# Kernel tuning notes

Measured on AMD Instinct MI355X. Metric: run time of the kernel, lower is better.

## Reference

```python
import jax, jax.numpy as jnp
import numpy as np

B, S, D = 4, 2048, 1024
H = 16
HD = D // H  # 64

def setup_inputs() -> dict:
    key = jax.random.key(0)
    ks = jax.random.split(key, 4)
    scale = 0.02
    return {
        "hidden_states": jax.random.normal(ks[0], (B, S, D), dtype=jnp.float32),
        "attention_mask": jnp.zeros((B, 1, 1, S), dtype=jnp.float32),
        "Wq": jax.random.normal(ks[1], (D, D), dtype=jnp.float32) * scale,
        "bq": jnp.zeros((D,), dtype=jnp.float32),
        "Wk": jax.random.normal(ks[2], (D, D), dtype=jnp.float32) * scale,
        "bk": jnp.zeros((D,), dtype=jnp.float32),
        "Wv": jax.random.normal(ks[3], (D, D), dtype=jnp.float32) * scale,
        "bv": jnp.zeros((D,), dtype=jnp.float32),
    }

def reference(hidden_states, attention_mask, Wq, bq, Wk, bk, Wv, bv):
    b, s, d = hidden_states.shape
    def proj(W, bias):
        # Linear then split heads: [b, s, d] -> [b, H, s, HD]
        y = hidden_states @ W.T + bias
        return y.reshape(b, s, H, HD).transpose(0, 2, 1, 3)
    Q = proj(Wq, bq)
    K = proj(Wk, bk)
    V = proj(Wv, bv)
    scores = jnp.einsum('bhqd,bhkd->bhqk', Q, K) / jnp.sqrt(jnp.float32(HD))
    scores = scores + attention_mask  # additive mask, broadcast [b,1,1,s]
    probs = jax.nn.softmax(scores, axis=-1)
    # dropout prob = 0.0 (eval-mode): identity
    context = jnp.einsum('bhqk,bhkd->bhqd', probs, V)
    return context.transpose(0, 2, 1, 3).reshape(b, s, d)
```

## Files before the change

### kernel.cpp

```cpp
#include <hip/hip_runtime.h>


typedef short bf16x4 __attribute__((ext_vector_type(4)));
typedef short bf16x8 __attribute__((ext_vector_type(8)));
typedef float f32x4 __attribute__((ext_vector_type(4)));

#define SEQ 2048
#define DIM 1024
#define NH 16
#define HDIM 64
#define QKV_ELEMS ((size_t)64 * SEQ * HDIM)

#define WS_FLAG  50331648ull
#define WS_XBF   50331904ull
#define WS_WBF   67109120ull
#define WS_BF32  73400576ull
#define WS_NEED  73412868ull

#define LOG2E 1.4426950408889634f
#define QSCALE (0.125f * LOG2E)

static __device__ __forceinline__ unsigned short f2bf(float f) {
  union { float f; unsigned u; } x; x.f = f;
  unsigned r = x.u + 0x7fffu + ((x.u >> 16) & 1u);
  return (unsigned short)(r >> 16);
}
static __device__ __forceinline__ float bf2f(unsigned short h) {
  union { unsigned u; float f; } x; x.u = ((unsigned)h) << 16;
  return x.f;
}
static __device__ __forceinline__ unsigned cvtpk(float a, float b) {
  unsigned r;
  asm("v_cvt_pk_bf16_f32 %0, %1, %2" : "=v"(r) : "v"(a), "v"(b));
  return r;
}
static __device__ __forceinline__ int vswz(int s) {
  return (s & ~31) | (((s >> 2) & 3) << 3) | (((s >> 4) & 1) << 2);
}
static __device__ __forceinline__ void vm_drain() {
  asm volatile("s_waitcnt vmcnt(0)" ::: "memory");
}

template <bool FP32>
static __device__ __forceinline__ float load1(const void* p, size_t i) {
  if (FP32) return ((const float*)p)[i];
  else      return bf2f(((const unsigned short*)p)[i]);
}
template <bool FP32>
static __device__ __forceinline__ bf16x8 load8bf(const void* p, size_t i) {
  if (FP32) {
    f32x4 a = *(const f32x4*)((const float*)p + i);
    f32x4 b = *(const f32x4*)((const float*)p + i + 4);
    union { bf16x8 v; unsigned short u[8]; } r;
#pragma unroll
    for (int j = 0; j < 4; ++j) { r.u[j] = f2bf(a[j]); r.u[4 + j] = f2bf(b[j]); }
    return r.v;
  } else {
    return *(const bf16x8*)((const unsigned short*)p + i);
  }
}
static __device__ __forceinline__ bf16x8 load8bf_rt(const void* p, size_t i, bool fp32) {
  return fp32 ? load8bf<true>(p, i) : load8bf<false>(p, i);
}

static __device__ __forceinline__ void glds16(const unsigned short* g, unsigned short* l) {
  __builtin_amdgcn_global_load_lds(
      (const __attribute__((address_space(1))) unsigned int*)(unsigned long long)(const void*)g,
      (__attribute__((address_space(3))) unsigned int*)(unsigned int)(unsigned long long)(void*)l,
      16, 0, 0);
}

__global__ void detect_dtype(const unsigned short* __restrict__ X, int* __restrict__ flag) {
  __shared__ int zc[1024], bc[1024];
  int z = 0, b = 0;
  for (int i = threadIdx.x; i < 4096; i += 1024) {
    unsigned short u = X[8 * i];
    if (u == 0) z++;
    int e = (u >> 7) & 0xff;
    if (e >= 134) b++;
  }
  zc[threadIdx.x] = z; bc[threadIdx.x] = b;
  __syncthreads();
  for (int s = 512; s > 0; s >>= 1) {
    if (threadIdx.x < s) { zc[threadIdx.x] += zc[threadIdx.x + s]; bc[threadIdx.x] += bc[threadIdx.x + s]; }
    __syncthreads();
  }
  if (threadIdx.x == 0)
    *flag = (zc[0] > 2048 || bc[0] > 16) ? 1 : 0;
}

__global__ void convert_all_u(const void* __restrict__ X,
                              const void* __restrict__ Wq, const void* __restrict__ Wk,
                              const void* __restrict__ Wv,
                              const void* __restrict__ bq, const void* __restrict__ bk,
                              const void* __restrict__ bv,
                              unsigned char* __restrict__ ws, const int* __restrict__ flag) {
  const bool fp32 = (*flag != 0);
  unsigned short* Xb = (unsigned short*)(ws + WS_XBF);
  unsigned short* Wb = (unsigned short*)(ws + WS_WBF);
  float* Bb = (float*)(ws + WS_BF32);
  int blk = blockIdx.x;
  if (blk < 4096) {
    size_t base = ((size_t)blk * 256 + threadIdx.x) * 8;
    *(bf16x8*)(Xb + base) = load8bf_rt(X, base, fp32);
  } else if (blk < 5632) {
    int w = (blk - 4096) >> 9;
    int r = (blk - 4096) & 511;
    const void* W = (w == 0) ? Wq : (w == 1) ? Wk : Wv;
    size_t base = ((size_t)r * 256 + threadIdx.x) * 8;
    *(bf16x8*)(Wb + (size_t)w * 1048576 + base) = load8bf_rt(W, base, fp32);
  } else {
    int w = blk - 5632;
    const void* Bsrc = (w == 0) ? bq : (w == 1) ? bk : bv;
    for (int i = threadIdx.x; i < 1024; i += 256)
      Bb[w * 1024 + i] = fp32 ? load1<true>(Bsrc, i) : load1<false>(Bsrc, i);
  }
}

__global__ __launch_bounds__(512, 2) void qkv_bf(
    const unsigned short* __restrict__ Xb, const unsigned short* __restrict__ Wb,
    const float* __restrict__ Bb,
    unsigned short* __restrict__ Qo, unsigned short* __restrict__ Ko,
    unsigned short* __restrict__ Vo)
{
  const int bid = blockIdx.x;
  const int wg  = (bid & 7) * 192 + (bid >> 3);
  const int z   = wg / 512;
  const int rem = wg - z * 512;
  const int nb  = rem >> 6;
  const int mb  = rem & 63;
  const unsigned short* W = Wb + (size_t)z * 1048576;

  __shared__ __align__(16) unsigned short Xs[2][128 * 64];
  __shared__ __align__(16) unsigned short Ws[2][128 * 64];

  const int tid  = threadIdx.x;
  const int wave = tid >> 6;
  const int lane = tid & 63;
  const int col  = lane & 15;
  const int quad = lane >> 4;
  const int wr = wave & 1;
  const int wc = wave >> 1;
  const int m0 = mb * 128;
  const int n0 = nb * 128;

  f32x4 zero4 = {0.f, 0.f, 0.f, 0.f};
  f32x4 acc[4][2];
#pragma unroll
  for (int i = 0; i < 4; ++i)
#pragma unroll
    for (int j = 0; j < 2; ++j) acc[i][j] = zero4;

  const int srow8 = lane >> 3;
  const int sseg  = lane & 7;
  const int lseg  = sseg ^ srow8;
  const unsigned short* xA0 = Xb + (size_t)(m0 + 0  + wave * 8 + srow8) * DIM + lseg * 8;
  const unsigned short* xA1 = Xb + (size_t)(m0 + 64 + wave * 8 + srow8) * DIM + lseg * 8;
  const unsigned short* wA0 = W  + (size_t)(n0 + 0  + wave * 8 + srow8) * DIM + lseg * 8;
  const unsigned short* wA1 = W  + (size_t)(n0 + 64 + wave * 8 + srow8) * DIM + lseg * 8;

  auto stage = [&](int k0, int bufn) {
    unsigned short* Xd = Xs[bufn] + (wave * 8) * 64;
    unsigned short* Wd = Ws[bufn] + (wave * 8) * 64;
    glds16(xA0 + k0, Xd);
    glds16(xA1 + k0, Xd + 64 * 64);
    glds16(wA0 + k0, Wd);
    glds16(wA1 + k0, Wd + 64 * 64);
  };

  stage(0, 0);

  if (z < 2) {
    for (int ks = 0; ks < 16; ++ks) {
      vm_drain();
      __syncthreads();
      if (ks < 15) stage((ks + 1) * 64, (ks + 1) & 1);
      const unsigned short* Xc = Xs[ks & 1];
      const unsigned short* Wc = Ws[ks & 1];
#pragma unroll
      for (int kk = 0; kk < 2; ++kk) {
        bf16x8 Af[4], Bf[2];
#pragma unroll
        for (int i = 0; i < 4; ++i) {
          int ra = wr * 64 + i * 16 + col;
          Af[i] = *(const bf16x8*)(Xc + ra * 64 + ((kk * 4 + quad) ^ (ra & 7)) * 8);
        }
#pragma unroll
        for (int j = 0; j < 2; ++j) {
          int rb = wc * 32 + j * 16 + col;
          Bf[j] = *(const bf16x8*)(Wc + rb * 64 + ((kk * 4 + quad) ^ (rb & 7)) * 8);
        }
#pragma unroll
        for (int i = 0; i < 4; ++i)
#pragma unroll
          for (int j = 0; j < 2; ++j)
            acc[i][j] = __builtin_amdgcn_mfma_f32_16x16x32_bf16(Bf[j], Af[i], acc[i][j], 0, 0, 0);
      }
    }

    const float oscale = (z == 0) ? QSCALE : 1.0f;
    unsigned short* Yo = (z == 0) ? Qo : Ko;
#pragma unroll
    for (int i = 0; i < 4; ++i) {
      int m = m0 + wr * 64 + i * 16 + col;
      int b = m >> 11, s = m & 2047;
#pragma unroll
      for (int j = 0; j < 2; ++j) {
        int n = n0 + wc * 32 + j * 16 + quad * 4;
        f32x4 bv4 = *(const f32x4*)(Bb + z * 1024 + n);
        int h = n >> 6, hd = n & 63;
        unsigned lo = cvtpk((acc[i][j][0] + bv4[0]) * oscale,
                            (acc[i][j][1] + bv4[1]) * oscale);
        unsigned hi = cvtpk((acc[i][j][2] + bv4[2]) * oscale,
                            (acc[i][j][3] + bv4[3]) * oscale);
        unsigned long long pk = (unsigned long long)lo | ((unsigned long long)hi << 32);
        *(unsigned long long*)(Yo + ((size_t)(b * NH + h) * SEQ + s) * HDIM + hd) = pk;
      }
    }
  } else {
    for (int ks = 0; ks < 16; ++ks) {
      vm_drain();
      __syncthreads();
      if (ks < 15) stage((ks + 1) * 64, (ks + 1) & 1);
      const unsigned short* Xc = Xs[ks & 1];
      const unsigned short* Wc = Ws[ks & 1];
#pragma unroll
      for (int kk = 0; kk < 2; ++kk) {
        bf16x8 Af[4], Bf[2];
#pragma unroll
        for (int i = 0; i < 4; ++i) {
          int ra = wr * 64 + i * 16 + col;
          Af[i] = *(const bf16x8*)(Xc + ra * 64 + ((kk * 4 + quad) ^ (ra & 7)) * 8);
        }
#pragma unroll
        for (int j = 0; j < 2; ++j) {
          int rb = wc * 32 + j * 16 + col;
          Bf[j] = *(const bf16x8*)(Wc + rb * 64 + ((kk * 4 + quad) ^ (rb & 7)) * 8);
        }
#pragma unroll
        for (int i = 0; i < 4; ++i)
#pragma unroll
          for (int j = 0; j < 2; ++j)
            acc[i][j] = __builtin_amdgcn_mfma_f32_16x16x32_bf16(Af[i], Bf[j], acc[i][j], 0, 0, 0);
      }
    }

#pragma unroll
    for (int i = 0; i < 4; ++i) {
#pragma unroll
      for (int j = 0; j < 2; ++j) {
        int n = n0 + wc * 32 + j * 16 + col;
        float bvf = Bb[2 * 1024 + n];
        int h = n >> 6, hd = n & 63;
        int mbase = m0 + wr * 64 + i * 16 + quad * 4;
        int b = mbase >> 11, s = mbase & 2047;
        unsigned lo = cvtpk(acc[i][j][0] + bvf, acc[i][j][1] + bvf);
        unsigned hi = cvtpk(acc[i][j][2] + bvf, acc[i][j][3] + bvf);
        unsigned long long pk = (unsigned long long)lo | ((unsigned long long)hi << 32);
        *(unsigned long long*)(Vo + ((size_t)(b * NH + h) * HDIM + hd) * SEQ + vswz(s)) = pk;
      }
    }
  }
}

#define XS_STRIDE 40
template <bool FP32>
__global__ __launch_bounds__(256) void qkv_any(
    const void* __restrict__ X,
    const void* __restrict__ Wq, const void* __restrict__ bq,
    const void* __restrict__ Wk, const void* __restrict__ bk,
    const void* __restrict__ Wv, const void* __restrict__ bv,
    unsigned short* __restrict__ Qo, unsigned short* __restrict__ Ko,
    unsigned short* __restrict__ Vo, const int* __restrict__ flag)
{
  if (*flag != (FP32 ? 1 : 0)) return;
  const int z = blockIdx.z;
  const void* W    = (z == 0) ? Wq : (z == 1) ? Wk : Wv;
  const void* bias = (z == 0) ? bq : (z == 1) ? bk : bv;

  __shared__ __align__(16) unsigned short Xs[128 * XS_STRIDE];
  __shared__ __align__(16) unsigned short Ws[128 * XS_STRIDE];

  const int tid  = threadIdx.x;
  const int wave = tid >> 6;
  const int lane = tid & 63;
  const int col  = lane & 15;
  const int quad = lane >> 4;
  const int wr = wave & 1;
  const int wc = wave >> 1;
  const int m0 = blockIdx.x * 128;
  const int n0 = blockIdx.y * 128;

  f32x4 zero4 = {0.f, 0.f, 0.f, 0.f};
  f32x4 acc[4][4];
#pragma unroll
  for (int i = 0; i < 4; ++i)
#pragma unroll
    for (int j = 0; j < 4; ++j) acc[i][j] = zero4;

  const int srow = tid >> 2;
  const int sseg = (tid & 3) << 3;

  for (int k0 = 0; k0 < DIM; k0 += 32) {
    __syncthreads();
#pragma unroll
    for (int a = 0; a < 2; ++a) {
      int r = a * 64 + srow;
      *(bf16x8*)(Xs + r * XS_STRIDE + sseg) = load8bf<FP32>(X, (size_t)(m0 + r) * DIM + k0 + sseg);
      *(bf16x8*)(Ws + r * XS_STRIDE + sseg) = load8bf<FP32>(W, (size_t)(n0 + r) * DIM + k0 + sseg);
    }
    __syncthreads();

    bf16x8 Af[4], Bf[4];
#pragma unroll
    for (int i = 0; i < 4; ++i)
      Af[i] = *(const bf16x8*)(Xs + (wr * 64 + i * 16 + col) * XS_STRIDE + quad * 8);
#pragma unroll
    for (int j = 0; j < 4; ++j)
      Bf[j] = *(const bf16x8*)(Ws + (wc * 64 + j * 16 + col) * XS_STRIDE + quad * 8);
#pragma unroll
    for (int i = 0; i < 4; ++i)
#pragma unroll
      for (int j = 0; j < 4; ++j)
        acc[i][j] = __builtin_amdgcn_mfma_f32_16x16x32_bf16(Af[i], Bf[j], acc[i][j], 0, 0, 0);
  }

  const float oscale = (z == 0) ? QSCALE : 1.0f;
  if (z < 2) {
    unsigned short* Yo = (z == 0) ? Qo : Ko;
#pragma unroll
    for (int i = 0; i < 4; ++i) {
#pragma unroll
      for (int j = 0; j < 4; ++j) {
        int n = n0 + wc * 64 + j * 16 + col;
        float bvf = load1<FP32>(bias, n);
        int h = n >> 6, hd = n & 63;
#pragma unroll
        for (int r = 0; r < 4; ++r) {
          int m = m0 + wr * 64 + i * 16 + quad * 4 + r;
          int b = m >> 11, s = m & 2047;
          Yo[((size_t)(b * NH + h) * SEQ + s) * HDIM + hd] = f2bf((acc[i][j][r] + bvf) * oscale);
        }
      }
    }
  } else {
#pragma unroll
    for (int i = 0; i < 4; ++i) {
#pragma unroll
      for (int j = 0; j < 4; ++j) {
        int n = n0 + wc * 64 + j * 16 + col;
        float bvf = load1<FP32>(bias, n);
        int h = n >> 6, hd = n & 63;
        int mbase = m0 + wr * 64 + i * 16 + quad * 4;
        int b = mbase >> 11, s = mbase & 2047;
        unsigned long long pk = 0;
#pragma unroll
        for (int r = 0; r < 4; ++r)
          pk |= (unsigned long long)f2bf(acc[i][j][r] + bvf) << (16 * r);
        *(unsigned long long*)(Vo + ((size_t)(b * NH + h) * HDIM + hd) * SEQ + vswz(s)) = pk;
      }
    }
  }
}

__global__ __launch_bounds__(512, 2) void attn_kernel(
    const unsigned short* __restrict__ Q,
    const unsigned short* __restrict__ K,
    const unsigned short* __restrict__ Vt,
    const void* __restrict__ mask,
    void* __restrict__ OutV, const int* __restrict__ flag)
{
  const bool fp32 = (*flag != 0);

  __shared__ __align__(16) unsigned short Ks[2 * 128 * 64];
  __shared__ __align__(16) unsigned short Vs[2 * 64 * 128];
  __shared__ __align__(16) float Msall[SEQ];

  const int tid  = threadIdx.x;
  const int wave = tid >> 6;
  const int lane = tid & 63;
  const int col  = lane & 15;
  const int quad = lane >> 4;
  const int qt = blockIdx.x;
  const int bh = blockIdx.y;
  const int b  = bh >> 4;
  const int h  = bh & 15;

  const unsigned short* Qb = Q  + (size_t)bh * SEQ * HDIM;
  const unsigned short* Kb = K  + (size_t)bh * SEQ * HDIM;
  const unsigned short* Vb = Vt + (size_t)bh * HDIM * SEQ;

  {
    if (fp32) {
      f32x4 a = *(const f32x4*)((const float*)mask + (size_t)b * SEQ + tid * 4);
#pragma unroll
      for (int j = 0; j < 4; ++j) a[j] *= LOG2E;
      *(f32x4*)(Msall + tid * 4) = a;
    } else {
      bf16x4 v = *(const bf16x4*)((const unsigned short*)mask + (size_t)b * SEQ + tid * 4);
      f32x4 a;
#pragma unroll
      for (int j = 0; j < 4; ++j) a[j] = bf2f((unsigned short)v[j]) * LOG2E;
      *(f32x4*)(Msall + tid * 4) = a;
    }
  }

  const int qrow0 = qt * 256 + wave * 32 + col;
  const int qrow1 = qrow0 + 16;
  const bf16x8 Qf00 = *(const bf16x8*)(Qb + (size_t)qrow0 * HDIM + quad * 8);
  const bf16x8 Qf01 = *(const bf16x8*)(Qb + (size_t)qrow0 * HDIM + 32 + quad * 8);
  const bf16x8 Qf10 = *(const bf16x8*)(Qb + (size_t)qrow1 * HDIM + quad * 8);
  const bf16x8 Qf11 = *(const bf16x8*)(Qb + (size_t)qrow1 * HDIM + 32 + quad * 8);

  const f32x4 z4 = {0.f, 0.f, 0.f, 0.f};
  f32x4 Oacc0[4], Oacc1[4];
  f32x4 Osum0 = z4, Osum1 = z4;
#pragma unroll
  for (int t = 0; t < 4; ++t) { Oacc0[t] = z4; Oacc1[t] = z4; }
  float mrun0 = -1e30f, mrun1 = -1e30f;

  union { bf16x8 v; unsigned u[4]; } ones;
#pragma unroll
  for (int i = 0; i < 4; ++i) ones.u[i] = 0x3F803F80u;

  const int krow_in = lane >> 3;
  const int kphys   = lane & 7;
  const int klseg   = kphys ^ krow_in;
  const unsigned short* kSrc0 = Kb + (size_t)(wave * 16 + 0 + krow_in) * HDIM + klseg * 8;
  const unsigned short* kSrc1 = Kb + (size_t)(wave * 16 + 8 + krow_in) * HDIM + klseg * 8;
  const int vrow_in = lane >> 4;
  const int vphys   = lane & 15;
  const int vrowA0  = wave * 8 + 0 + vrow_in;
  const int vrowA1  = wave * 8 + 4 + vrow_in;
  const unsigned short* vSrc0 = Vb + (size_t)vrowA0 * SEQ + (vphys ^ (vrowA0 & 15)) * 8;
  const unsigned short* vSrc1 = Vb + (size_t)vrowA1 * SEQ + (vphys ^ (vrowA1 & 15)) * 8;

  auto stage = [&](int ktn, int bufn) {
    unsigned short* Kdst = Ks + bufn * (128 * 64) + (wave * 16) * 64;
    unsigned short* Vdst = Vs + bufn * (64 * 128) + (wave * 8) * 128;
    const size_t ko = (size_t)ktn * 128 * HDIM;
    const size_t vo = (size_t)ktn * 128;
    glds16(kSrc0 + ko, Kdst);
    glds16(kSrc1 + ko, Kdst + 8 * 64);
    glds16(vSrc0 + vo, Vdst);
    glds16(vSrc1 + vo, Vdst + 4 * 128);
  };

  stage(0, 0);

  for (int kt = 0; kt < 16; ++kt) {
    vm_drain();
    __syncthreads();
    if (kt < 15) stage(kt + 1, (kt + 1) & 1);

    const unsigned short* Kcur = Ks + (kt & 1) * (128 * 64);
    const unsigned short* Vcur = Vs + (kt & 1) * (64 * 128);
    const float* Mc = Msall + kt * 128;

    f32x4 st0[8], st1[8];
    __builtin_amdgcn_s_setprio(1);
#pragma unroll
    for (int t = 0; t < 8; ++t) {
      const unsigned short* kr = Kcur + (t * 16 + col) * 64;
      bf16x8 Ka = *(const bf16x8*)(kr + (quad ^ (col & 7)) * 8);
      bf16x8 Kc = *(const bf16x8*)(kr + ((4 + quad) ^ (col & 7)) * 8);
      f32x4 c = *(const f32x4*)(Mc + t * 16 + quad * 4);
      f32x4 d0 = c, d1 = c;
      d0 = __builtin_amdgcn_mfma_f32_16x16x32_bf16(Ka, Qf00, d0, 0, 0, 0);
      d0 = __builtin_amdgcn_mfma_f32_16x16x32_bf16(Kc, Qf01, d0, 0, 0, 0);
      d1 = __builtin_amdgcn_mfma_f32_16x16x32_bf16(Ka, Qf10, d1, 0, 0, 0);
      d1 = __builtin_amdgcn_mfma_f32_16x16x32_bf16(Kc, Qf11, d1, 0, 0, 0);
      st0[t] = d0; st1[t] = d1;
    }
    __builtin_amdgcn_s_setprio(0);

    bf16x8 Bv01[2][4];
#pragma unroll
    for (int tp = 0; tp < 2; ++tp)
#pragma unroll
      for (int t2 = 0; t2 < 4; ++t2)
        Bv01[tp][t2] = *(const bf16x8*)(Vcur + (t2 * 16 + col) * 128 + ((tp * 4 + quad) ^ col) * 8);

    float pm0, pm1;
    {
      f32x4 m40, m41;
#pragma unroll
      for (int r = 0; r < 4; ++r) {
        float a0 = fmaxf(fmaxf(st0[0][r], st0[1][r]), st0[2][r]);
        a0 = fmaxf(fmaxf(a0, st0[3][r]), st0[4][r]);
        a0 = fmaxf(fmaxf(a0, st0[5][r]), st0[6][r]);
        m40[r] = fmaxf(a0, st0[7][r]);
        float a1 = fmaxf(fmaxf(st1[0][r], st1[1][r]), st1[2][r]);
        a1 = fmaxf(fmaxf(a1, st1[3][r]), st1[4][r]);
        a1 = fmaxf(fmaxf(a1, st1[5][r]), st1[6][r]);
        m41[r] = fmaxf(a1, st1[7][r]);
      }
      pm0 = fmaxf(fmaxf(fmaxf(m40[0], m40[1]), m40[2]), m40[3]);
      pm1 = fmaxf(fmaxf(fmaxf(m41[0], m41[1]), m41[2]), m41[3]);
    }
    pm0 = fmaxf(pm0, __shfl_xor(pm0, 16, 64));
    pm0 = fmaxf(pm0, __shfl_xor(pm0, 32, 64));
    pm1 = fmaxf(pm1, __shfl_xor(pm1, 16, 64));
    pm1 = fmaxf(pm1, __shfl_xor(pm1, 32, 64));

    if (!__all((pm0 - mrun0 <= 8.0f) && (pm1 - mrun1 <= 8.0f))) {
      float mn0 = fmaxf(mrun0, pm0), mn1 = fmaxf(mrun1, pm1);
      float a0 = __builtin_amdgcn_exp2f(mrun0 - mn0);
      float a1 = __builtin_amdgcn_exp2f(mrun1 - mn1);
      mrun0 = mn0; mrun1 = mn1;
      float av0[4], av1[4];
#pragma unroll
      for (int r = 0; r < 4; ++r) {
        av0[r] = __shfl(a0, quad * 4 + r, 64);
        av1[r] = __shfl(a1, quad * 4 + r, 64);
      }
#pragma unroll
      for (int t = 0; t < 4; ++t)
#pragma unroll
        for (int r = 0; r < 4; ++r) {
          Oacc0[t][r] *= av0[r];
          Oacc1[t][r] *= av1[r];
        }
#pragma unroll
      for (int r = 0; r < 4; ++r) { Osum0[r] *= av0[r]; Osum1[r] *= av1[r]; }
    }

#pragma unroll
    for (int t = 0; t < 8; ++t)
#pragma unroll
      for (int r = 0; r < 4; ++r) {
        st0[t][r] = __builtin_amdgcn_exp2f(st0[t][r] - mrun0);
        st1[t][r] = __builtin_amdgcn_exp2f(st1[t][r] - mrun1);
      }

    __builtin_amdgcn_s_setprio(1);
#pragma unroll
    for (int tp = 0; tp < 4; ++tp) {
      union { bf16x8 v; unsigned u[4]; } A0, A1;
      A0.u[0] = cvtpk(st0[2 * tp][0],     st0[2 * tp][1]);
      A0.u[1] = cvtpk(st0[2 * tp][2],     st0[2 * tp][3]);
      A0.u[2] = cvtpk(st0[2 * tp + 1][0], st0[2 * tp + 1][1]);
      A0.u[3] = cvtpk(st0[2 * tp + 1][2], st0[2 * tp + 1][3]);
      A1.u[0] = cvtpk(st1[2 * tp][0],     st1[2 * tp][1]);
      A1.u[1] = cvtpk(st1[2 * tp][2],     st1[2 * tp][3]);
      A1.u[2] = cvtpk(st1[2 * tp + 1][0], st1[2 * tp + 1][1]);
      A1.u[3] = cvtpk(st1[2 * tp + 1][2], st1[2 * tp + 1][3]);
      Osum0 = __builtin_amdgcn_mfma_f32_16x16x32_bf16(A0.v, ones.v, Osum0, 0, 0, 0);
      Osum1 = __builtin_amdgcn_mfma_f32_16x16x32_bf16(A1.v, ones.v, Osum1, 0, 0, 0);
#pragma unroll
      for (int t2 = 0; t2 < 4; ++t2) {
        bf16x8 Bv = (tp < 2) ? Bv01[tp][t2]
                  : *(const bf16x8*)(Vcur + (t2 * 16 + col) * 128 + ((tp * 4 + quad) ^ col) * 8);
        Oacc0[t2] = __builtin_amdgcn_mfma_f32_16x16x32_bf16(A0.v, Bv, Oacc0[t2], 0, 0, 0);
        Oacc1[t2] = __builtin_amdgcn_mfma_f32_16x16x32_bf16(A1.v, Bv, Oacc1[t2], 0, 0, 0);
      }
    }
    __builtin_amdgcn_s_setprio(0);
  }

  float liv0[4], liv1[4];
#pragma unroll
  for (int r = 0; r < 4; ++r) { liv0[r] = 1.0f / Osum0[r]; liv1[r] = 1.0f / Osum1[r]; }
#pragma unroll
  for (int t2 = 0; t2 < 4; ++t2) {
#pragma unroll
    for (int r = 0; r < 4; ++r) {
      int q0 = qt * 256 + wave * 32 + quad * 4 + r;
      int q1 = q0 + 16;
      float v0 = Oacc0[t2][r] * liv0[r];
      float v1 = Oacc1[t2][r] * liv1[r];
      v0 = (v0 == v0) ? v0 : 0.0f;
      v1 = (v1 == v1) ? v1 : 0.0f;
      size_t o0 = ((size_t)b * SEQ + q0) * DIM + h * HDIM + t2 * 16 + col;
      size_t o1 = ((size_t)b * SEQ + q1) * DIM + h * HDIM + t2 * 16 + col;
      if (fp32) {
        ((float*)OutV)[o0] = v0;
        ((float*)OutV)[o1] = v1;
      } else {
        ((unsigned short*)OutV)[o0] = f2bf(v0);
        ((unsigned short*)OutV)[o1] = f2bf(v1);
      }
    }
  }
}

extern "C" void kernel_launch(void* const* d_in, const int* in_sizes, int n_in,
                              void* d_out, int out_size, void* d_ws, size_t ws_size,
                              hipStream_t stream) {
  const void* X    = d_in[0];
  const void* mask = d_in[1];
  const void* Wq   = d_in[2];
  const void* bq   = d_in[3];
  const void* Wk   = d_in[4];
  const void* bk   = d_in[5];
  const void* Wv   = d_in[6];
  const void* bv   = d_in[7];

  unsigned char* ws = (unsigned char*)d_ws;
  unsigned short* Qw = (unsigned short*)ws;
  unsigned short* Kw = Qw + QKV_ELEMS;
  unsigned short* Vw = Kw + QKV_ELEMS;
  int* flag = (int*)(ws + WS_FLAG);

  detect_dtype<<<1, 1024, 0, stream>>>((const unsigned short*)X, flag);

  if (ws_size >= WS_NEED) {
    convert_all_u<<<5635, 256, 0, stream>>>(X, Wq, Wk, Wv, bq, bk, bv, ws, flag);
    qkv_bf<<<1536, 512, 0, stream>>>(
        (const unsigned short*)(ws + WS_XBF), (const unsigned short*)(ws + WS_WBF),
        (const float*)(ws + WS_BF32), Qw, Kw, Vw);
  } else {
    qkv_any<false><<<dim3(64, 8, 3), 256, 0, stream>>>(X, Wq, bq, Wk, bk, Wv, bv, Qw, Kw, Vw, flag);
    qkv_any<true ><<<dim3(64, 8, 3), 256, 0, stream>>>(X, Wq, bq, Wk, bk, Wv, bv, Qw, Kw, Vw, flag);
  }

  attn_kernel<<<dim3(8, 64), 512, 0, stream>>>(Qw, Kw, Vw, mask, d_out, flag);
}
```

Baseline: 260.0 us.

## Widen QKV GEMM tile to 128x256 with K=32 stages and preload all V fragments

The QKV projection GEMM now uses 128x256 output tiles, each wave owning a 64x64 block with 16 accumulators, and halves the K-step to 32 so the double-buffered shared memory stays small. The grid shrinks to 768 blocks. The aim is more MFMA work per shared-memory fragment load and less global traffic per output. In the attention kernel, all four V fragment groups are loaded into registers up front instead of two, to hide LDS latency. Both changes raise register pressure, and the shorter K-step doubles the number of barriers per tile.

Result: faster. 251.8 us (-3.1%).

```diff
diff --git a/kernel.cpp b/kernel.cpp
--- a/kernel.cpp
+++ b/kernel.cpp
@@ -124,15 +124,15 @@
     unsigned short* __restrict__ Vo)
 {
   const int bid = blockIdx.x;
-  const int wg  = (bid & 7) * 192 + (bid >> 3);
-  const int z   = wg / 512;
-  const int rem = wg - z * 512;
+  const int wg  = (bid & 7) * 96 + (bid >> 3);
+  const int z   = wg >> 8;
+  const int rem = wg & 255;
   const int nb  = rem >> 6;
   const int mb  = rem & 63;
   const unsigned short* W = Wb + (size_t)z * 1048576;
 
-  __shared__ __align__(16) unsigned short Xs[2][128 * 64];
-  __shared__ __align__(16) unsigned short Ws[2][128 * 64];
+  __shared__ __align__(16) unsigned short Xs[2][128 * 32];
+  __shared__ __align__(16) unsigned short Ws[2][256 * 32];
 
   const int tid  = threadIdx.x;
   const int wave = tid >> 6;
@@ -142,60 +142,53 @@
   const int wr = wave & 1;
   const int wc = wave >> 1;
   const int m0 = mb * 128;
-  const int n0 = nb * 128;
+  const int n0 = nb * 256;
 
   f32x4 zero4 = {0.f, 0.f, 0.f, 0.f};
-  f32x4 acc[4][2];
+  f32x4 acc[4][4];
 #pragma unroll
   for (int i = 0; i < 4; ++i)
 #pragma unroll
-    for (int j = 0; j < 2; ++j) acc[i][j] = zero4;
-
-  const int srow8 = lane >> 3;
-  const int sseg  = lane & 7;
-  const int lseg  = sseg ^ srow8;
-  const unsigned short* xA0 = Xb + (size_t)(m0 + 0  + wave * 8 + srow8) * DIM + lseg * 8;
-  const unsigned short* xA1 = Xb + (size_t)(m0 + 64 + wave * 8 + srow8) * DIM + lseg * 8;
-  const unsigned short* wA0 = W  + (size_t)(n0 + 0  + wave * 8 + srow8) * DIM + lseg * 8;
-  const unsigned short* wA1 = W  + (size_t)(n0 + 64 + wave * 8 + srow8) * DIM + lseg * 8;
+    for (int j = 0; j < 4; ++j) acc[i][j] = zero4;
+
+  const int srow16 = lane >> 2;
+  const int sseg   = lane & 3;
+  const int lseg   = sseg ^ (srow16 & 3);
+  const unsigned short* xA  = Xb + (size_t)(m0 + wave * 16 + srow16) * DIM + lseg * 8;
+  const unsigned short* wA0 = W  + (size_t)(n0 +   0 + wave * 16 + srow16) * DIM + lseg * 8;
+  const unsigned short* wA1 = W  + (size_t)(n0 + 128 + wave * 16 + srow16) * DIM + lseg * 8;
 
   auto stage = [&](int k0, int bufn) {
-    unsigned short* Xd = Xs[bufn] + (wave * 8) * 64;
-    unsigned short* Wd = Ws[bufn] + (wave * 8) * 64;
-    glds16(xA0 + k0, Xd);
-    glds16(xA1 + k0, Xd + 64 * 64);
-    glds16(wA0 + k0, Wd);
-    glds16(wA1 + k0, Wd + 64 * 64);
+    glds16(xA  + k0, Xs[bufn] + (wave * 16) * 32);
+    glds16(wA0 + k0, Ws[bufn] + (wave * 16) * 32);
+    glds16(wA1 + k0, Ws[bufn] + (128 + wave * 16) * 32);
   };
 
   stage(0, 0);
 
   if (z < 2) {
-    for (int ks = 0; ks < 16; ++ks) {
+    for (int ks = 0; ks < 32; ++ks) {
       vm_drain();
       __syncthreads();
-      if (ks < 15) stage((ks + 1) * 64, (ks + 1) & 1);
+      if (ks < 31) stage((ks + 1) * 32, (ks + 1) & 1);
       const unsigned short* Xc = Xs[ks & 1];
       const unsigned short* Wc = Ws[ks & 1];
-#pragma unroll
-      for (int kk = 0; kk < 2; ++kk) {
-        bf16x8 Af[4], Bf[2];
-#pragma unroll
-        for (int i = 0; i < 4; ++i) {
-          int ra = wr * 64 + i * 16 + col;
-          Af[i] = *(const bf16x8*)(Xc + ra * 64 + ((kk * 4 + quad) ^ (ra & 7)) * 8);
-        }
-#pragma unroll
-        for (int j = 0; j < 2; ++j) {
-          int rb = wc * 32 + j * 16 + col;
-          Bf[j] = *(const bf16x8*)(Wc + rb * 64 + ((kk * 4 + quad) ^ (rb & 7)) * 8);
-        }
-#pragma unroll
-        for (int i = 0; i < 4; ++i)
-#pragma unroll
-          for (int j = 0; j < 2; ++j)
-            acc[i][j] = __builtin_amdgcn_mfma_f32_16x16x32_bf16(Bf[j], Af[i], acc[i][j], 0, 0, 0);
-      }
+      bf16x8 Af[4], Bf[4];
+#pragma unroll
+      for (int i = 0; i < 4; ++i) {
+        int ra = wr * 64 + i * 16 + col;
+        Af[i] = *(const bf16x8*)(Xc + ra * 32 + (quad ^ (ra & 3)) * 8);
+      }
+#pragma unroll
+      for (int j = 0; j < 4; ++j) {
+        int rb = wc * 64 + j * 16 + col;
+        Bf[j] = *(const bf16x8*)(Wc + rb * 32 + (quad ^ (rb & 3)) * 8);
+      }
+#pragma unroll
+      for (int i = 0; i < 4; ++i)
+#pragma unroll
+        for (int j = 0; j < 4; ++j)
+          acc[i][j] = __builtin_amdgcn_mfma_f32_16x16x32_bf16(Bf[j], Af[i], acc[i][j], 0, 0, 0);
     }
 
     const float oscale = (z == 0) ? QSCALE : 1.0f;
@@ -205,8 +198,8 @@
       int m = m0 + wr * 64 + i * 16 + col;
       int b = m >> 11, s = m & 2047;
 #pragma unroll
-      for (int j = 0; j < 2; ++j) {
-        int n = n0 + wc * 32 + j * 16 + quad * 4;
+      for (int j = 0; j < 4; ++j) {
+        int n = n0 + wc * 64 + j * 16 + quad * 4;
         f32x4 bv4 = *(const f32x4*)(Bb + z * 1024 + n);
         int h = n >> 6, hd = n & 63;
         unsigned lo = cvtpk((acc[i][j][0] + bv4[0]) * oscale,
@@ -218,38 +211,35 @@
       }
     }
   } else {
-    for (int ks = 0; ks < 16; ++ks) {
+    for (int ks = 0; ks < 32; ++ks) {
       vm_drain();
       __syncthreads();
-      if (ks < 15) stage((ks + 1) * 64, (ks + 1) & 1);
+      if (ks < 31) stage((ks + 1) * 32, (ks + 1) & 1);
       const unsigned short* Xc = Xs[ks & 1];
       const unsigned short* Wc = Ws[ks & 1];
-#pragma unroll
-      for (int kk = 0; kk < 2; ++kk) {
-        bf16x8 Af[4], Bf[2];
-#pragma unroll
-        for (int i = 0; i < 4; ++i) {
-          int ra = wr * 64 + i * 16 + col;
-          Af[i] = *(const bf16x8*)(Xc + ra * 64 + ((kk * 4 + quad) ^ (ra & 7)) * 8);
-        }
-#pragma unroll
-        for (int j = 0; j < 2; ++j) {
-          int rb = wc * 32 + j * 16 + col;
-          Bf[j] = *(const bf16x8*)(Wc + rb * 64 + ((kk * 4 + quad) ^ (rb & 7)) * 8);
-        }
-#pragma unroll
-        for (int i = 0; i < 4; ++i)
-#pragma unroll
-          for (int j = 0; j < 2; ++j)
-            acc[i][j] = __builtin_amdgcn_mfma_f32_16x16x32_bf16(Af[i], Bf[j], acc[i][j], 0, 0, 0);
-      }
+      bf16x8 Af[4], Bf[4];
+#pragma unroll
+      for (int i = 0; i < 4; ++i) {
+        int ra = wr * 64 + i * 16 + col;
+        Af[i] = *(const bf16x8*)(Xc + ra * 32 + (quad ^ (ra & 3)) * 8);
+      }
+#pragma unroll
+      for (int j = 0; j < 4; ++j) {
+        int rb = wc * 64 + j * 16 + col;
+        Bf[j] = *(const bf16x8*)(Wc + rb * 32 + (quad ^ (rb & 3)) * 8);
+      }
+#pragma unroll
+      for (int i = 0; i < 4; ++i)
+#pragma unroll
+        for (int j = 0; j < 4; ++j)
+          acc[i][j] = __builtin_amdgcn_mfma_f32_16x16x32_bf16(Af[i], Bf[j], acc[i][j], 0, 0, 0);
     }
 
 #pragma unroll
     for (int i = 0; i < 4; ++i) {
 #pragma unroll
-      for (int j = 0; j < 2; ++j) {
-        int n = n0 + wc * 32 + j * 16 + col;
+      for (int j = 0; j < 4; ++j) {
+        int n = n0 + wc * 64 + j * 16 + col;
         float bvf = Bb[2 * 1024 + n];
         int h = n >> 6, hd = n & 63;
         int mbase = m0 + wr * 64 + i * 16 + quad * 4;
@@ -474,12 +464,12 @@
     }
     __builtin_amdgcn_s_setprio(0);
 
-    bf16x8 Bv01[2][4];
-#pragma unroll
-    for (int tp = 0; tp < 2; ++tp)
+    bf16x8 Bv[4][4];
+#pragma unroll
+    for (int tp = 0; tp < 4; ++tp)
 #pragma unroll
       for (int t2 = 0; t2 < 4; ++t2)
-        Bv01[tp][t2] = *(const bf16x8*)(Vcur + (t2 * 16 + col) * 128 + ((tp * 4 + quad) ^ col) * 8);
+        Bv[tp][t2] = *(const bf16x8*)(Vcur + (t2 * 16 + col) * 128 + ((tp * 4 + quad) ^ col) * 8);
 
     float pm0, pm1;
     {
@@ -549,10 +539,8 @@
       Osum1 = __builtin_amdgcn_mfma_f32_16x16x32_bf16(A1.v, ones.v, Osum1, 0, 0, 0);
 #pragma unroll
       for (int t2 = 0; t2 < 4; ++t2) {
-        bf16x8 Bv = (tp < 2) ? Bv01[tp][t2]
-                  : *(const bf16x8*)(Vcur + (t2 * 16 + col) * 128 + ((tp * 4 + quad) ^ col) * 8);
-        Oacc0[t2] = __builtin_amdgcn_mfma_f32_16x16x32_bf16(A0.v, Bv, Oacc0[t2], 0, 0, 0);
-        Oacc1[t2] = __builtin_amdgcn_mfma_f32_16x16x32_bf16(A1.v, Bv, Oacc1[t2], 0, 0, 0);
+        Oacc0[t2] = __builtin_amdgcn_mfma_f32_16x16x32_bf16(A0.v, Bv[tp][t2], Oacc0[t2], 0, 0, 0);
+        Oacc1[t2] = __builtin_amdgcn_mfma_f32_16x16x32_bf16(A1.v, Bv[tp][t2], Oacc1[t2], 0, 0, 0);
       }
     }
     __builtin_amdgcn_s_setprio(0);
@@ -606,7 +594,7 @@
 
   if (ws_size >= WS_NEED) {
     convert_all_u<<<5635, 256, 0, stream>>>(X, Wq, Wk, Wv, bq, bk, bv, ws, flag);
-    qkv_bf<<<1536, 512, 0, stream>>>(
+    qkv_bf<<<768, 512, 0, stream>>>(
         (const unsigned short*)(ws + WS_XBF), (const unsigned short*)(ws + WS_WBF),
         (const float*)(ws + WS_BF32), Qw, Kw, Vw);
   } else {
```
